# Optimization experiments

Measured on AMD Instinct MI355X. Metric: run time of the kernel, lower is better.

The kernel has to match this reference:

```python
import jax, jax.numpy as jnp
import numpy as np
import math

B, S, H = 2, 2048, 2048
NQ, NKV, HD = 16, 4, 128
THETA = 10000.0


def rotate_half(x):
    x1, x2 = jnp.split(x, 2, axis=-1)
    return jnp.concatenate([-x2, x1], axis=-1)


def rope_cos_sin(position_ids, dim, base, dtype):
    # inv_freq: (dim/2,)
    inv_freq = 1.0 / (base ** (jnp.arange(0, dim, 2, dtype=jnp.float32) / dim))
    freqs = position_ids.astype(jnp.float32)[..., None] * inv_freq  # (B, S, dim/2)
    emb = jnp.concatenate([freqs, freqs], axis=-1)  # (B, S, dim)
    return jnp.cos(emb).astype(dtype), jnp.sin(emb).astype(dtype)


def setup_inputs() -> dict:
    key = jax.random.key(0)
    ks = jax.random.split(key, 5)
    hidden_states = jax.random.normal(ks[0], (B, S, H), dtype=jnp.float32)
    position_ids = jnp.broadcast_to(jnp.arange(S, dtype=jnp.int32)[None, :], (B, S))
    sc = 0.02
    wq = jax.random.normal(ks[1], (NQ * HD, H), dtype=jnp.float32) * sc
    wk = jax.random.normal(ks[2], (NKV * HD, H), dtype=jnp.float32) * sc
    wv = jax.random.normal(ks[3], (NKV * HD, H), dtype=jnp.float32) * sc
    wo = jax.random.normal(ks[4], (H, NQ * HD), dtype=jnp.float32) * sc
    return {"hidden_states": hidden_states, "position_ids": position_ids,
            "wq": wq, "wk": wk, "wv": wv, "wo": wo}


def reference(hidden_states, position_ids, wq, wk, wv, wo):
    b, s, _ = hidden_states.shape
    n_rep = NQ // NKV
    # QKV projections (no bias)
    q = (hidden_states @ wq.T).reshape(b, s, NQ, HD).transpose(0, 2, 1, 3)   # (b, nq, s, hd)
    k = (hidden_states @ wk.T).reshape(b, s, NKV, HD).transpose(0, 2, 1, 3)  # (b, nkv, s, hd)
    v = (hidden_states @ wv.T).reshape(b, s, NKV, HD).transpose(0, 2, 1, 3)
    # RoPE (full rotary, partial_rotary_factor == 1.0)
    cos, sin = rope_cos_sin(position_ids, HD, THETA, q.dtype)  # (b, s, hd)
    cos = cos[:, None, :, :]
    sin = sin[:, None, :, :]
    q = q * cos + rotate_half(q) * sin
    k = k * cos + rotate_half(k) * sin
    # repeat_kv for GQA: (b, nkv, s, hd) -> (b, nq, s, hd)
    k = jnp.repeat(k, n_rep, axis=1)
    v = jnp.repeat(v, n_rep, axis=1)
    # scores (b, nq, s, s)
    scores = jnp.einsum('bhqd,bhkd->bhqk', q, k) / math.sqrt(HD)
    causal = jnp.triu(jnp.full((s, s), -jnp.inf, dtype=scores.dtype), k=1)
    scores = scores + causal
    probs = jax.nn.softmax(scores.astype(jnp.float32), axis=-1).astype(q.dtype)
    out = jnp.einsum('bhqk,bhkd->bhqd', probs, v)  # (b, nq, s, hd)
    out = out.transpose(0, 2, 1, 3).reshape(b, s, NQ * HD)
    return out @ wo.T
```

## Files before the change

kernel.cpp:

```cpp
#include <hip/hip_runtime.h>
#include <hip/hip_bf16.h>
#include <cstdint>

typedef unsigned short u16;
typedef __attribute__((ext_vector_type(4))) float f32x4;
typedef __attribute__((ext_vector_type(8))) short s16x8;
typedef __attribute__((ext_vector_type(4))) unsigned int u32x4;
typedef __attribute__((ext_vector_type(2))) unsigned int u32x2;
typedef __attribute__((ext_vector_type(4))) unsigned short u16x4;

#define MFMA16(a, b, c) __builtin_amdgcn_mfma_f32_16x16x32_bf16(a, b, c, 0, 0, 0)
#define GLOAD16(g, l) __builtin_amdgcn_global_load_lds((const __attribute__((address_space(1))) void*)(g), (__attribute__((address_space(3))) void*)(l), 16, 0, 0)

__device__ __forceinline__ u16 f2bf(float f) {
    union { float f; uint32_t u; } v{f};
    uint32_t r = v.u + 0x7FFF + ((v.u >> 16) & 1);
    return (u16)(r >> 16);
}
__device__ __forceinline__ float bf2f(u16 b) {
    union { uint32_t u; float f; } v;
    v.u = ((uint32_t)b) << 16;
    return v.f;
}

__global__ void cast_f32_bf16(const float* __restrict__ in, u16* __restrict__ out, int n4) {
    int i = blockIdx.x * 256 + threadIdx.x;
    if (i >= n4) return;
    float4 f = ((const float4*)in)[i];
    u16x4 o = { f2bf(f.x), f2bf(f.y), f2bf(f.z), f2bf(f.w) };
    ((u16x4*)out)[i] = o;
}

__global__ void rope_table_k(const int* __restrict__ pos, float* __restrict__ ct, float* __restrict__ st) {
    int i = blockIdx.x * 256 + threadIdx.x;
    int j = i & 63;
    int bs = i >> 6;
    float p = (float)pos[bs];
    float invf = powf(10000.0f, -(float)j * (1.0f / 64.0f));
    float ang = p * invf;
    ct[i] = cosf(ang);
    st[i] = sinf(ang);
}

template <int FUSE>
__global__ __launch_bounds__(256) void gemm_bt(const u16* __restrict__ A, const u16* __restrict__ Bw,
                                               float* __restrict__ C, int M, int N, int K,
                                               const float* __restrict__ ct, const float* __restrict__ st,
                                               u16* __restrict__ Qb, u16* __restrict__ Kb,
                                               u16* __restrict__ Vb) {
    __shared__ u16 Sh[128 * 128];
    u16* As = Sh;
    u16* Bs = Sh + 8192;
    const int tid = threadIdx.x;
    const int lane = tid & 63, wid = tid >> 6;
    const int g = lane >> 4, r = lane & 15;

    const int gx = gridDim.x, nwg = gx * gridDim.y;
    int lid = blockIdx.y * gx + blockIdx.x;
    int swz = (lid % 8) * (nwg / 8) + lid / 8;
    const int bxi = swz % gx, byi = swz / gx;

    const size_t bm = (size_t)byi * 128, bn = (size_t)bxi * 128;
    const int wr = (wid >> 1) * 64, wc = (wid & 1) * 64;

    const int srow = wid * 32 + (lane >> 3);
    const int schunk = (lane & 7) ^ ((lane >> 3) & 7);
    const u16* aSrc = A + (bm + srow) * (size_t)K + schunk * 8;
    const u16* bSrc = Bw + (bn + srow) * (size_t)K + schunk * 8;
    u16* aDst = As + wid * 2048;
    u16* bDst = Bs + wid * 2048;

    f32x4 acc[4][4] = {};
    for (int kt = 0; kt < K; kt += 64) {
#pragma unroll
        for (int j = 0; j < 4; ++j) {
            GLOAD16(aSrc + (size_t)(j * 8) * K + kt, aDst + j * 512);
            GLOAD16(bSrc + (size_t)(j * 8) * K + kt, bDst + j * 512);
        }
        __syncthreads();
        s16x8 af[4][2], bfr[4][2];
#pragma unroll
        for (int m = 0; m < 4; ++m)
#pragma unroll
            for (int kk = 0; kk < 2; ++kk) {
                int rowa = wr + m * 16 + r;
                af[m][kk] = *(const s16x8*)(As + rowa * 64 + (((kk * 4 + g) ^ (rowa & 7)) << 3));
                int rowb = wc + m * 16 + r;
                bfr[m][kk] = *(const s16x8*)(Bs + rowb * 64 + (((kk * 4 + g) ^ (rowb & 7)) << 3));
            }
#pragma unroll
        for (int m = 0; m < 4; ++m)
#pragma unroll
            for (int n = 0; n < 4; ++n) {
                acc[m][n] = MFMA16(af[m][0], bfr[n][0], acc[m][n]);
                acc[m][n] = MFMA16(af[m][1], bfr[n][1], acc[m][n]);
            }
        __syncthreads();
    }
    if (FUSE == 0) {
#pragma unroll
        for (int m = 0; m < 4; ++m)
#pragma unroll
            for (int n = 0; n < 4; ++n)
#pragma unroll
                for (int i = 0; i < 4; ++i) {
                    size_t row = bm + wr + m * 16 + g * 4 + i;
                    size_t col = bn + wc + n * 16 + r;
                    C[row * N + col] = acc[m][n][i];
                }
        return;
    }
#pragma unroll
    for (int m = 0; m < 4; ++m)
#pragma unroll
        for (int n = 0; n < 4; ++n)
#pragma unroll
            for (int i = 0; i < 4; ++i) {
                int rowl = wr + m * 16 + g * 4 + i;
                int col = wc + n * 16 + r;
                int c4 = col >> 3;
                *(u16*)((char*)Sh + rowl * 256 + (((c4 ^ (rowl & 15))) << 4) + ((col & 7) << 1)) =
                    f2bf(acc[m][n][i]);
            }
    __syncthreads();
    if (tid < 128) {
        const int rowl = tid;
        const size_t tok = bm + rowl;
        const int b = (int)(tok >> 11), s = (int)(tok & 2047);
        const int hb = bxi;
        u16* dst;
        if (hb < 16)      dst = Qb + (((size_t)(b * 16 + hb) * 2048 + s) << 7);
        else if (hb < 20) dst = Kb + (((size_t)(b * 4 + (hb - 16)) * 2048 + s) << 7);
        else              dst = Vb + (((size_t)(b * 4 + (hb - 20)) * 2048 + s) << 7);
        const char* tb = (const char*)Sh + rowl * 256;
        if (hb < 20) {
            const float* ctr = ct + tok * 64;
            const float* str = st + tok * 64;
#pragma unroll
            for (int c4 = 0; c4 < 8; ++c4) {
                u32x4 lo4 = *(const u32x4*)(tb + ((c4 ^ (rowl & 15)) << 4));
                u32x4 hi4 = *(const u32x4*)(tb + (((c4 + 8) ^ (rowl & 15)) << 4));
                const u16* lo = (const u16*)&lo4;
                const u16* hi = (const u16*)&hi4;
                u16x4 o0, o1, o2, o3;
                u16* olo[2] = { (u16*)&o0, (u16*)&o1 };
                u16* ohi[2] = { (u16*)&o2, (u16*)&o3 };
#pragma unroll
                for (int j = 0; j < 8; ++j) {
                    float c = ctr[c4 * 8 + j], sn = str[c4 * 8 + j];
                    float xl = bf2f(lo[j]), xh = bf2f(hi[j]);
                    olo[j >> 2][j & 3] = f2bf(xl * c - xh * sn);
                    ohi[j >> 2][j & 3] = f2bf(xh * c + xl * sn);
                }
                *(u16x4*)(dst + c4 * 8) = o0;
                *(u16x4*)(dst + c4 * 8 + 4) = o1;
                *(u16x4*)(dst + 64 + c4 * 8) = o2;
                *(u16x4*)(dst + 64 + c4 * 8 + 4) = o3;
            }
        } else {
#pragma unroll
            for (int c4 = 0; c4 < 16; ++c4) {
                u32x4 v4 = *(const u32x4*)(tb + ((c4 ^ (rowl & 15)) << 4));
                *(u32x4*)(dst + c4 * 8) = v4;
            }
        }
    }
}

__global__ __launch_bounds__(256, 2) void attn_k(const u16* __restrict__ Qb, const u16* __restrict__ Kb,
                                                 const u16* __restrict__ Vb, u16* __restrict__ Ob) {
    __shared__ char smem[49152];
    u16* Ksh = (u16*)smem;
    u16* Vts = (u16*)(smem + 16384);
    char* Pall = smem + 32768;
    const int tid = threadIdx.x;
    const int lane = tid & 63, w = tid >> 6;
    const int g = lane >> 4, r = lane & 15;

    const int lid = blockIdx.y * gridDim.x + blockIdx.x;
    const int cpy = lid >> 8, p = lid & 255;
    const int bh = p & 31;
    const int qblk = cpy ? (7 - (p >> 5)) : ((p >> 5) + 8);

    const int b = bh >> 4, h = bh & 15;
    const int hkv = h >> 2;
    const int q0 = qblk * 128;
    const u16* Qh = Qb + ((size_t)(b * 16 + h) << 18);
    const u16* Kh = Kb + ((size_t)(b * 4 + hkv) << 18);
    const u16* Vh = Vb + ((size_t)(b * 4 + hkv) << 18);

    s16x8 qf[2][4];
#pragma unroll
    for (int qq = 0; qq < 2; ++qq)
#pragma unroll
        for (int c = 0; c < 4; ++c)
            qf[qq][c] = *(const s16x8*)(Qh + (size_t)(q0 + qq * 64 + w * 16 + r) * 128 + c * 32 + g * 8);

    f32x4 o[2][8] = {};
    float mrun[2] = {-1e30f, -1e30f};
    float lrun[2] = {0.f, 0.f};
    const int fmax[2] = { q0 + w * 16 + 15, q0 + 64 + w * 16 + 15 };

    const int ntiles = 2 * qblk + 2;
    const int krow0 = tid >> 4, kch = tid & 15;
    const int vdc = tid & 15, vkvp = tid >> 4;

    u32x4 kpr[4], var[2], vbr[2];
#pragma unroll
    for (int it = 0; it < 4; ++it)
        kpr[it] = *(const u32x4*)(Kh + (size_t)(krow0 + it * 16) * 128 + kch * 8);
#pragma unroll
    for (int it = 0; it < 2; ++it) {
        int kv2 = (vkvp + it * 16) * 2;
        var[it] = *(const u32x4*)(Vh + (size_t)kv2 * 128 + vdc * 8);
        vbr[it] = *(const u32x4*)(Vh + (size_t)(kv2 + 1) * 128 + vdc * 8);
    }

    for (int t = 0; t < ntiles; ++t) {
        const int kv0 = t * 64;
        __syncthreads();
#pragma unroll
        for (int it = 0; it < 4; ++it) {
            int row = krow0 + it * 16;
            *(u32x4*)((char*)Ksh + row * 256 + ((kch ^ (row & 7)) << 4)) = kpr[it];
        }
#pragma unroll
        for (int it = 0; it < 2; ++it) {
            int kv2 = (vkvp + it * 16) * 2;
            const u16* p0 = (const u16*)&var[it];
            const u16* p1 = (const u16*)&vbr[it];
#pragma unroll
            for (int j = 0; j < 8; ++j) {
                int d = vdc * 8 + j;
                unsigned int val = (unsigned int)p0[j] | ((unsigned int)p1[j] << 16);
                *(unsigned int*)((char*)Vts +
                    ((d * 128 + kv2 * 2) ^ ((((d & 7) ^ ((d >> 3) & 7))) << 4))) = val;
            }
        }
        __syncthreads();
        if (t + 1 < ntiles) {
            const int kn = kv0 + 64;
#pragma unroll
            for (int it = 0; it < 4; ++it)
                kpr[it] = *(const u32x4*)(Kh + (size_t)(kn + krow0 + it * 16) * 128 + kch * 8);
#pragma unroll
            for (int it = 0; it < 2; ++it) {
                int kv2 = kn + (vkvp + it * 16) * 2;
                var[it] = *(const u32x4*)(Vh + (size_t)kv2 * 128 + vdc * 8);
                vbr[it] = *(const u32x4*)(Vh + (size_t)(kv2 + 1) * 128 + vdc * 8);
            }
        }
        f32x4 st4[2][4];
#pragma unroll
        for (int ts = 0; ts < 4; ++ts) {
            int row = ts * 16 + r;
            s16x8 kf[4];
#pragma unroll
            for (int c = 0; c < 4; ++c)
                kf[c] = *(const s16x8*)((const char*)Ksh + row * 256 + (((c * 4 + g) ^ (row & 7)) << 4));
            f32x4 a0 = {}, a1 = {};
            if (kv0 <= fmax[0])
#pragma unroll
                for (int c = 0; c < 4; ++c) a0 = MFMA16(kf[c], qf[0][c], a0);
            if (kv0 <= fmax[1])
#pragma unroll
                for (int c = 0; c < 4; ++c) a1 = MFMA16(kf[c], qf[1][c], a1);
            st4[0][ts] = a0;
            st4[1][ts] = a1;
        }
#pragma unroll
        for (int qq = 0; qq < 2; ++qq) {
            if (kv0 > fmax[qq]) continue;
            const int qg = q0 + qq * 64 + w * 16 + r;
            float sv[16];
            float mtile = -1e30f;
#pragma unroll
            for (int ts = 0; ts < 4; ++ts)
#pragma unroll
                for (int i = 0; i < 4; ++i) {
                    int kvg = kv0 + ts * 16 + g * 4 + i;
                    float s = st4[qq][ts][i] * 0.08838834764831845f;
                    s = (kvg > qg) ? -1e30f : s;
                    sv[ts * 4 + i] = s;
                    mtile = fmaxf(mtile, s);
                }
            mtile = fmaxf(mtile, __shfl_xor(mtile, 16));
            mtile = fmaxf(mtile, __shfl_xor(mtile, 32));
            float mnew = fmaxf(mrun[qq], mtile);
            float corr = __expf(mrun[qq] - mnew);
            float psum = 0.f;
            unsigned int pw[8];
#pragma unroll
            for (int ts = 0; ts < 4; ++ts) {
                float p0 = __expf(sv[ts * 4 + 0] - mnew);
                float p1 = __expf(sv[ts * 4 + 1] - mnew);
                float p2 = __expf(sv[ts * 4 + 2] - mnew);
                float p3 = __expf(sv[ts * 4 + 3] - mnew);
                psum += (p0 + p1) + (p2 + p3);
                pw[ts * 2 + 0] = (unsigned int)f2bf(p0) | ((unsigned int)f2bf(p1) << 16);
                pw[ts * 2 + 1] = (unsigned int)f2bf(p2) | ((unsigned int)f2bf(p3) << 16);
            }
            psum += __shfl_xor(psum, 16);
            psum += __shfl_xor(psum, 32);
            lrun[qq] = lrun[qq] * corr + psum;
            mrun[qq] = mnew;
#pragma unroll
            for (int dsb = 0; dsb < 8; ++dsb)
#pragma unroll
                for (int i = 0; i < 4; ++i) o[qq][dsb][i] *= corr;
            char* pbase = Pall + (w * 2 + qq) * 2048;
#pragma unroll
            for (int ts = 0; ts < 4; ++ts) {
                int chunk = (ts * 2 + (g >> 1)) ^ (r & 7);
                u32x2 val = { pw[ts * 2], pw[ts * 2 + 1] };
                *(u32x2*)(pbase + r * 128 + chunk * 16 + (g & 1) * 8) = val;
            }
        }
        asm volatile("s_waitcnt lgkmcnt(0)" ::: "memory");
#pragma unroll
        for (int c = 0; c < 2; ++c) {
            s16x8 vf[8];
#pragma unroll
            for (int dsb = 0; dsb < 8; ++dsb) {
                int d = dsb * 16 + r;
                vf[dsb] = *(const s16x8*)((const char*)Vts + d * 128 +
                    ((((c * 4 + g) ^ (d & 7) ^ ((d >> 3) & 7))) << 4));
            }
#pragma unroll
            for (int qq = 0; qq < 2; ++qq) {
                if (kv0 > fmax[qq]) continue;
                s16x8 pf = *(const s16x8*)(Pall + (w * 2 + qq) * 2048 + r * 128 +
                                           (((c * 4 + g) ^ (r & 7)) << 4));
#pragma unroll
                for (int dsb = 0; dsb < 8; ++dsb)
                    o[qq][dsb] = MFMA16(vf[dsb], pf, o[qq][dsb]);
            }
        }
    }
    __syncthreads();
#pragma unroll
    for (int qq = 0; qq < 2; ++qq) {
        float linv = 1.0f / lrun[qq];
        char* obase = smem + (w << 13) + (qq << 12);
#pragma unroll
        for (int dsb = 0; dsb < 8; ++dsb)
#pragma unroll
            for (int i = 0; i < 4; ++i) {
                int d = dsb * 16 + g * 4 + i;
                *(u16*)(obase + r * 256 + d * 2) = f2bf(o[qq][dsb][i] * linv);
            }
    }
    asm volatile("s_waitcnt lgkmcnt(0)" ::: "memory");
    const int rr = lane >> 2, cbo = (lane & 3) * 32;
#pragma unroll
    for (int qq = 0; qq < 2; ++qq) {
        char* obase = smem + (w << 13) + (qq << 12);
        size_t oidx = ((size_t)b * 2048 + q0 + qq * 64 + w * 16 + rr) * 2048 + h * 128 + cbo;
#pragma unroll
        for (int p2 = 0; p2 < 4; ++p2) {
            u32x4 vv = *(const u32x4*)(obase + rr * 256 + cbo * 2 + p2 * 16);
            *(u32x4*)(Ob + oidx + p2 * 8) = vv;
        }
    }
}

extern "C" void kernel_launch(void* const* d_in, const int* in_sizes, int n_in,
                              void* d_out, int out_size, void* d_ws, size_t ws_size,
                              hipStream_t stream) {
    const float* hidden = (const float*)d_in[0];
    const int* pos = (const int*)d_in[1];
    const float* wq = (const float*)d_in[2];
    const float* wk = (const float*)d_in[3];
    const float* wv = (const float*)d_in[4];
    const float* wo = (const float*)d_in[5];
    float* out = (float*)d_out;

    char* ws = (char*)d_ws;
    size_t off = 0;
    auto alloc = [&](size_t bytes) { char* p = ws + off; off += (bytes + 255) & ~255ULL; return p; };
    u16* Xb   = (u16*)alloc(8388608ULL * 2);
    u16* WB   = (u16*)alloc(6291456ULL * 2);
    u16* WoB  = (u16*)alloc(4194304ULL * 2);
    u16* Qb   = (u16*)alloc(8388608ULL * 2);
    u16* Kb   = (u16*)alloc(2097152ULL * 2);
    u16* Vb   = (u16*)alloc(2097152ULL * 2);
    u16* Ab   = (u16*)alloc(8388608ULL * 2);
    float* ctab = (float*)alloc(262144ULL * 4);
    float* stab = (float*)alloc(262144ULL * 4);

    cast_f32_bf16<<<8192, 256, 0, stream>>>(hidden, Xb, 2097152);
    cast_f32_bf16<<<4096, 256, 0, stream>>>(wq, WB, 1048576);
    cast_f32_bf16<<<1024, 256, 0, stream>>>(wk, WB + 4194304, 262144);
    cast_f32_bf16<<<1024, 256, 0, stream>>>(wv, WB + 5242880, 262144);
    cast_f32_bf16<<<4096, 256, 0, stream>>>(wo, WoB, 1048576);
    rope_table_k<<<1024, 256, 0, stream>>>(pos, ctab, stab);
    gemm_bt<1><<<dim3(24, 32), 256, 0, stream>>>(Xb, WB, nullptr, 4096, 3072, 2048,
                                                 ctab, stab, Qb, Kb, Vb);
    attn_k<<<dim3(16, 32), 256, 0, stream>>>(Qb, Kb, Vb, Ab);
    gemm_bt<0><<<dim3(16, 32), 256, 0, stream>>>(Ab, WoB, out, 4096, 2048, 2048,
                                                 nullptr, nullptr, nullptr, nullptr, nullptr);
}
```

Baseline: 249.6 us.

## Store V transposed from QKV projection epilogue to simplify attention V staging

The QKV GEMM epilogue now writes V in a transposed (head_dim-major, token-contiguous) layout, gathering columns out of the swizzled shared tile. The attention kernel can then load V tiles with plain 16-byte vector loads and store them straight into the swizzled transposed LDS buffer. This replaces the per-element 32-bit interleave stores it used before. The cost moves to the epilogue, which now does scalar 2-byte LDS reads per element, and the change couples the two kernels through the new V layout.

```diff
diff --git a/kernel.cpp b/kernel.cpp
--- a/kernel.cpp
+++ b/kernel.cpp
@@ -8,6 +8,7 @@
 typedef __attribute__((ext_vector_type(4))) unsigned int u32x4;
 typedef __attribute__((ext_vector_type(2))) unsigned int u32x2;
 typedef __attribute__((ext_vector_type(4))) unsigned short u16x4;
+typedef __attribute__((ext_vector_type(8))) unsigned short u16x8;
 
 #define MFMA16(a, b, c) __builtin_amdgcn_mfma_f32_16x16x32_bf16(a, b, c, 0, 0, 0)
 #define GLOAD16(g, l) __builtin_amdgcn_global_load_lds((const __attribute__((address_space(1))) void*)(g), (__attribute__((address_space(3))) void*)(l), 16, 0, 0)
@@ -124,16 +125,15 @@
             }
     __syncthreads();
     if (tid < 128) {
-        const int rowl = tid;
-        const size_t tok = bm + rowl;
-        const int b = (int)(tok >> 11), s = (int)(tok & 2047);
         const int hb = bxi;
-        u16* dst;
-        if (hb < 16)      dst = Qb + (((size_t)(b * 16 + hb) * 2048 + s) << 7);
-        else if (hb < 20) dst = Kb + (((size_t)(b * 4 + (hb - 16)) * 2048 + s) << 7);
-        else              dst = Vb + (((size_t)(b * 4 + (hb - 20)) * 2048 + s) << 7);
-        const char* tb = (const char*)Sh + rowl * 256;
         if (hb < 20) {
+            const int rowl = tid;
+            const size_t tok = bm + rowl;
+            const int b = (int)(tok >> 11), s = (int)(tok & 2047);
+            u16* dst;
+            if (hb < 16) dst = Qb + (((size_t)(b * 16 + hb) * 2048 + s) << 7);
+            else         dst = Kb + (((size_t)(b * 4 + (hb - 16)) * 2048 + s) << 7);
+            const char* tb = (const char*)Sh + rowl * 256;
             const float* ctr = ct + tok * 64;
             const float* str = st + tok * 64;
 #pragma unroll
@@ -158,10 +158,21 @@
                 *(u16x4*)(dst + 64 + c4 * 8 + 4) = o3;
             }
         } else {
-#pragma unroll
-            for (int c4 = 0; c4 < 16; ++c4) {
-                u32x4 v4 = *(const u32x4*)(tb + ((c4 ^ (rowl & 15)) << 4));
-                *(u32x4*)(dst + c4 * 8) = v4;
+            const int d = tid;
+            const size_t tok0 = bm;
+            const int b = (int)(tok0 >> 11), s0 = (int)(tok0 & 2047);
+            u16* dst = Vb + (size_t)(b * 4 + (hb - 20)) * 262144 + (size_t)d * 2048 + s0;
+            const int dslot = d >> 3, dbyte = (d & 7) << 1;
+#pragma unroll
+            for (int jb = 0; jb < 16; ++jb) {
+                u16x8 v;
+#pragma unroll
+                for (int jj = 0; jj < 8; ++jj) {
+                    int s = jb * 8 + jj;
+                    v[jj] = *(const u16*)((const char*)Sh + s * 256 +
+                                          (((dslot ^ (s & 15))) << 4) + dbyte);
+                }
+                *(u16x8*)(dst + jb * 8) = v;
             }
         }
     }
@@ -203,17 +214,15 @@
 
     const int ntiles = 2 * qblk + 2;
     const int krow0 = tid >> 4, kch = tid & 15;
-    const int vdc = tid & 15, vkvp = tid >> 4;
-
-    u32x4 kpr[4], var[2], vbr[2];
+
+    u32x4 kpr[4], vpr[4];
 #pragma unroll
     for (int it = 0; it < 4; ++it)
         kpr[it] = *(const u32x4*)(Kh + (size_t)(krow0 + it * 16) * 128 + kch * 8);
 #pragma unroll
-    for (int it = 0; it < 2; ++it) {
-        int kv2 = (vkvp + it * 16) * 2;
-        var[it] = *(const u32x4*)(Vh + (size_t)kv2 * 128 + vdc * 8);
-        vbr[it] = *(const u32x4*)(Vh + (size_t)(kv2 + 1) * 128 + vdc * 8);
+    for (int it = 0; it < 4; ++it) {
+        int task = tid + it * 256;
+        vpr[it] = *(const u32x4*)(Vh + (size_t)(task >> 3) * 2048 + (task & 7) * 8);
     }
 
     for (int t = 0; t < ntiles; ++t) {
@@ -225,17 +234,10 @@
             *(u32x4*)((char*)Ksh + row * 256 + ((kch ^ (row & 7)) << 4)) = kpr[it];
         }
 #pragma unroll
-        for (int it = 0; it < 2; ++it) {
-            int kv2 = (vkvp + it * 16) * 2;
-            const u16* p0 = (const u16*)&var[it];
-            const u16* p1 = (const u16*)&vbr[it];
-#pragma unroll
-            for (int j = 0; j < 8; ++j) {
-                int d = vdc * 8 + j;
-                unsigned int val = (unsigned int)p0[j] | ((unsigned int)p1[j] << 16);
-                *(unsigned int*)((char*)Vts +
-                    ((d * 128 + kv2 * 2) ^ ((((d & 7) ^ ((d >> 3) & 7))) << 4))) = val;
-            }
+        for (int it = 0; it < 4; ++it) {
+            int task = tid + it * 256;
+            int d = task >> 3, ch = task & 7;
+            *(u32x4*)((char*)Vts + d * 128 + ((ch ^ (d & 7) ^ ((d >> 3) & 7)) << 4)) = vpr[it];
         }
         __syncthreads();
         if (t + 1 < ntiles) {
@@ -244,10 +246,9 @@
             for (int it = 0; it < 4; ++it)
                 kpr[it] = *(const u32x4*)(Kh + (size_t)(kn + krow0 + it * 16) * 128 + kch * 8);
 #pragma unroll
-            for (int it = 0; it < 2; ++it) {
-                int kv2 = kn + (vkvp + it * 16) * 2;
-                var[it] = *(const u32x4*)(Vh + (size_t)kv2 * 128 + vdc * 8);
-                vbr[it] = *(const u32x4*)(Vh + (size_t)(kv2 + 1) * 128 + vdc * 8);
+            for (int it = 0; it < 4; ++it) {
+                int task = tid + it * 256;
+                vpr[it] = *(const u32x4*)(Vh + (size_t)(task >> 3) * 2048 + kn + (task & 7) * 8);
             }
         }
         f32x4 st4[2][4];
```

After: 259.9 us. 1.04x slower.
